# Kernel tuning notes

Measured on AMD Instinct MI355X. Metric: run time of the kernel, lower is better.

Reference implementation:

```python
import jax, jax.numpy as jnp
import numpy as np

SEQ_LEN = 16384
TAG_SIZE = 1024
NEG_INF = -10000.0


def setup_inputs() -> dict:
    key = jax.random.key(0)
    k1, k2, k3 = jax.random.split(key, 3)
    feats = jax.random.normal(k1, (SEQ_LEN, TAG_SIZE), dtype=jnp.float32)
    transitions = jax.random.normal(k2, (TAG_SIZE, TAG_SIZE), dtype=jnp.float32)
    tags = jax.random.randint(k3, (SEQ_LEN,), 0, 1022, dtype=jnp.int64)
    return {
        "feats": feats,
        "transitions": transitions,
        "tags": tags,
        "start_idx": 1022,
        "stop_idx": 1023,
    }


def reference(feats, transitions, tags, start_idx, stop_idx):
    tag_size = transitions.shape[0]

    # --- forward algorithm (log partition function) ---
    init = jnp.full((tag_size,), NEG_INF, dtype=feats.dtype).at[start_idx].set(0.0)

    def step(fv, feat):
        # next_tag_var[j, i] = fv[i] + transitions[j, i] + feat[j]
        new = jax.nn.logsumexp(fv[None, :] + transitions, axis=1) + feat
        return new, None

    fv, _ = jax.lax.scan(step, init, feats)
    forward_score = jax.nn.logsumexp(fv + transitions[stop_idx])  # scalar

    # --- gold score (faithful to original, incl. feats[tags[i+1]] row-indexing) ---
    tags_ext = jnp.concatenate([jnp.array([start_idx], dtype=tags.dtype), tags])
    trans_sum = jnp.sum(transitions[tags_ext[1:], tags_ext[:-1]])  # scalar
    # original adds feats[tags[i+1]] (a full row, [tag_size]) each step -> vector score
    emit_sum = jnp.sum(feats[tags_ext[1:]], axis=0)  # [tag_size]
    gold_score = trans_sum + emit_sum + transitions[stop_idx, tags_ext[-1]]  # [tag_size]

    return forward_score - gold_score  # [tag_size], matches broadcast in torch code
```

## Files before the change

### kernel.cpp

```cpp
#include <hip/hip_runtime.h>
#include <stdint.h>

#define LOG2E_F 1.4426950408889634f
#define LN2_D   0.6931471805599453
#define SEQLEN  16384
#define NTAGS   1024
#define TPB     512
#define NGROUP  32
#define GPB     8
#define ROWS    128
#define CPG     32
#define LSEG    32
#define KCH     512
#define COFF    13.0f
#define GUARD_MAX 100000
#define PARW    (CPG * 256)

typedef float f32x2 __attribute__((ext_vector_type(2)));
typedef float f32x4 __attribute__((ext_vector_type(4)));
typedef uint32_t u32;
typedef uint64_t u64;

#define REP4(M, B)   M(B) M((B)+1) M((B)+2) M((B)+3)
#define REP16(M, B)  REP4(M, B) REP4(M, (B)+4) REP4(M, (B)+8) REP4(M, (B)+12)
#define REP32(M, B)  REP16(M, B) REP16(M, (B)+16)

#if __has_builtin(__builtin_amdgcn_cvt_pk_fp8_f32) && __has_builtin(__builtin_amdgcn_cvt_pk_f32_fp8)
__device__ __forceinline__ u32 pack4_fp8(float x0, float x1, float x2, float x3) {
    int v = __builtin_amdgcn_cvt_pk_fp8_f32(x0, x1, 0, false);
    v = __builtin_amdgcn_cvt_pk_fp8_f32(x2, x3, v, true);
    return (u32)v;
}
__device__ __forceinline__ float dec8(u32 b) {
    f32x2 r = (f32x2)__builtin_amdgcn_cvt_pk_f32_fp8((int)(b & 0xFFu), false);
    return r.x;
}
#else
__device__ __forceinline__ u32 enc1_fp8(float x) {
    if (x >= 448.f) return 0x7Eu;
    if (x < 0.015625f) { int m = (int)(x * 512.f + 0.5f); return (u32)m; }
    u32 u = __float_as_uint(x);
    u += 0x7FFFFu + ((u >> 20) & 1u);
    int e32 = (int)(u >> 23) - 127;
    if (e32 > 8) return 0x7Eu;
    return (u32)(((e32 + 7) << 3) | ((u >> 20) & 7u));
}
__device__ __forceinline__ u32 pack4_fp8(float x0, float x1, float x2, float x3) {
    return enc1_fp8(x0) | (enc1_fp8(x1) << 8) | (enc1_fp8(x2) << 16) | (enc1_fp8(x3) << 24);
}
__device__ __forceinline__ float dec8(u32 b) {
    b &= 0xFFu;
    u32 e = (b >> 3) & 0xFu, m = b & 7u;
    if (e == 0) return (float)m * 0.001953125f;
    return __uint_as_float(((e + 120u) << 23) | (m << 20));
}
#endif

__global__ void crf_prep_k(u32* __restrict__ flags,
                           const float* __restrict__ feats, const int* __restrict__ tags,
                           float* __restrict__ part, const float* __restrict__ trans,
                           const int* __restrict__ start_p, float* __restrict__ tsum) {
    __shared__ int tg[2048];
    __shared__ float red[256];
    const int b = blockIdx.x, tid = threadIdx.x;
    if (b == 0) {
        for (int i = tid; i < NGROUP * 16; i += 256)
            __hip_atomic_store(&flags[i], 0xFFFFu, __ATOMIC_RELAXED, __HIP_MEMORY_SCOPE_AGENT);
    } else if (b < 33) {
        const int bb = b - 1, cch = bb >> 2, jb = bb & 3;
        for (int q = tid; q < 2048; q += 256) tg[q] = tags[cch * 2048 + q];
        __syncthreads();
        const int j = jb * 256 + tid;
        float acc = 0.f;
#pragma unroll 8
        for (int k = 0; k < 2048; ++k) acc += feats[(size_t)tg[k] * NTAGS + j];
        part[cch * NTAGS + j] = acc;
    } else {
        const int start = *start_p;
        float acc = 0.f;
        for (int k = 0; k < 64; ++k) {
            const int t = tid * 64 + k;
            const int prev = (t == 0) ? start : tags[t - 1];
            acc += trans[(size_t)tags[t] * NTAGS + prev];
        }
        red[tid] = acc;
        __syncthreads();
        for (int s = 128; s > 0; s >>= 1) { if (tid < s) red[tid] += red[tid + s]; __syncthreads(); }
        if (tid == 0) *tsum = red[0];
    }
}

__global__ __launch_bounds__(TPB, 1) void crf_scan_k(
    const float* __restrict__ feats, const float* __restrict__ trans,
    u32* __restrict__ wbufs, u32* __restrict__ flags, double* __restrict__ Ssum)
{
    extern __shared__ uint2 wBf[];
    __shared__ u32 cmaxb[2][CPG];
    __shared__ float fbx[8][16][17];
    __shared__ int okf, deadf;

    const int tid = threadIdx.x;
    const int l = tid & 63, wv = tid >> 6;
    const int g = blockIdx.x & 31, rank = blockIdx.x >> 5;
    const int bwd = g >> 4, gl = g & 15;
    const int row0 = rank * ROWS;
    const int pc = tid >> 4, pq = tid & 15;
    const int myc = l & 15, h = l >> 4;
    const int growA = row0 + wv * 16 + myc;
    const int growD = row0 + wv * 16 + h * 4;
    u32* wgrp = wbufs + (size_t)g * (2 * PARW);
    u32* fgrp = flags + g * 16;

    if (tid == 0) { okf = 1; deadf = 0; }
    double Sacc = bwd ? 3.0 : 0.0;

    for (int f = tid; f < CPG * 32; f += TPB) {
        const int c = f >> 5, q = f & 31;
        u32 pk;
        if (!bwd) pk = 0x38383838u;
        else {
            const int t = (gl * CPG + c) * LSEG + LSEG - 1;
            const int j0 = row0 + 4 * q;
            const float4 fv = *(const float4*)&feats[(size_t)t * NTAGS + j0];
            pk = pack4_fp8(exp2f(fv.x * LOG2E_F - 3.0f), exp2f(fv.y * LOG2E_F - 3.0f),
                           exp2f(fv.z * LOG2E_F - 3.0f), exp2f(fv.w * LOG2E_F - 3.0f));
        }
        __hip_atomic_store(&wgrp[c * 256 + (row0 >> 2) + q], pk,
                           __ATOMIC_RELAXED, __HIP_MEMORY_SCOPE_AGENT);
    }
    asm volatile("s_waitcnt vmcnt(0)" ::: "memory");
    __syncthreads();
    if (tid == 0)
        __hip_atomic_store(&fgrp[0 * 8 + rank], 0u, __ATOMIC_RELAXED, __HIP_MEMORY_SCOPE_AGENT);

    u64 afr[32];
#define STG(KK) { \
        const int kb = (KK) * 32 + h * 8; \
        float x0,x1,x2,x3,x4,x5,x6,x7; \
        if (!bwd) { \
            const float4 t0 = *(const float4*)&trans[(size_t)growA * NTAGS + kb]; \
            const float4 t1 = *(const float4*)&trans[(size_t)growA * NTAGS + kb + 4]; \
            x0=t0.x; x1=t0.y; x2=t0.z; x3=t0.w; x4=t1.x; x5=t1.y; x6=t1.z; x7=t1.w; \
        } else { \
            x0 = trans[(size_t)(kb+0)*NTAGS + growA]; x1 = trans[(size_t)(kb+1)*NTAGS + growA]; \
            x2 = trans[(size_t)(kb+2)*NTAGS + growA]; x3 = trans[(size_t)(kb+3)*NTAGS + growA]; \
            x4 = trans[(size_t)(kb+4)*NTAGS + growA]; x5 = trans[(size_t)(kb+5)*NTAGS + growA]; \
            x6 = trans[(size_t)(kb+6)*NTAGS + growA]; x7 = trans[(size_t)(kb+7)*NTAGS + growA]; \
        } \
        const u32 lo = pack4_fp8(exp2f(x0*LOG2E_F), exp2f(x1*LOG2E_F), exp2f(x2*LOG2E_F), exp2f(x3*LOG2E_F)); \
        const u32 hi = pack4_fp8(exp2f(x4*LOG2E_F), exp2f(x5*LOG2E_F), exp2f(x6*LOG2E_F), exp2f(x7*LOG2E_F)); \
        afr[KK] = (u64)lo | ((u64)hi << 32); }
    REP32(STG, 0)
#undef STG

    {
        float av0,av1,av2,av3,av4,av5,av6,av7, bv0,bv1,bv2,bv3,bv4,bv5,bv6,bv7;
#define TV(I) { const int k = h*8 + (I); \
        const float a_ = (float)((myc + k) & 3); \
        const float b_ = (float)(((k ^ myc) & 3) + 1); \
        if ((I)==0){av0=a_;bv0=b_;} if ((I)==1){av1=a_;bv1=b_;} \
        if ((I)==2){av2=a_;bv2=b_;} if ((I)==3){av3=a_;bv3=b_;} \
        if ((I)==4){av4=a_;bv4=b_;} if ((I)==5){av5=a_;bv5=b_;} \
        if ((I)==6){av6=a_;bv6=b_;} if ((I)==7){av7=a_;bv7=b_;} }
        TV(0) TV(1) TV(2) TV(3) TV(4) TV(5) TV(6) TV(7)
#undef TV
        const u64 at = (u64)pack4_fp8(av0,av1,av2,av3) | ((u64)pack4_fp8(av4,av5,av6,av7) << 32);
        const u64 bt = (u64)pack4_fp8(bv0,bv1,bv2,bv3) | ((u64)pack4_fp8(bv4,bv5,bv6,bv7) << 32);
        f32x4 dz = {0.f, 0.f, 0.f, 0.f};
        dz = __builtin_amdgcn_mfma_f32_16x16x32_fp8_fp8((long)at, (long)bt, dz, 0, 0, 0);
        bool good = true;
#pragma unroll
        for (int v = 0; v < 4; ++v) {
            const int row = h * 4 + v;
            float e = 0.f;
            for (int k = 0; k < 32; ++k)
                e += (float)(((row + k) & 3) * (((k ^ myc) & 3) + 1));
            good = good && (dz[v] == e);
        }
        if (!good) okf = 0;
    }
    __syncthreads();
    const bool fb = (okf == 0);

    for (int tau = 0; tau < LSEG; ++tau) {
        const int p = tau & 1;
        const u32 tag = (u32)tau;

        float4 ffa = make_float4(0.f,0.f,0.f,0.f), ffb = make_float4(0.f,0.f,0.f,0.f);
        {
            int t = -1;
            if (!bwd) t = tau; else if (tau <= LSEG - 2) t = LSEG - 2 - tau;
            if (t >= 0) {
                const int ca = gl * CPG + myc;
                ffa = *(const float4*)&feats[(size_t)(ca * LSEG + t) * NTAGS + growD];
                ffb = *(const float4*)&feats[(size_t)((ca + 16) * LSEG + t) * NTAGS + growD];
            }
        }

        if (wv == 0) {
            int guard = 0;
            u32 fv = tag;
            for (;;) {
                if (l < GPB)
                    fv = __hip_atomic_load(&fgrp[p * 8 + l],
                                           __ATOMIC_RELAXED, __HIP_MEMORY_SCOPE_AGENT);
                if (__all(fv == tag)) break;
                if (++guard > GUARD_MAX) { deadf = 1; break; }
            }
        }
        __syncthreads();
        if (deadf) break;

        u32 w[16];
        {
            const u32* pp = wgrp + p * PARW + pc * 256 + pq * 16;
#pragma unroll
            for (int q = 0; q < 8; ++q) {
                const u64 v = __hip_atomic_load((const u64*)(pp + 2 * q),
                                                __ATOMIC_RELAXED, __HIP_MEMORY_SCOPE_AGENT);
                w[2 * q] = (u32)v; w[2 * q + 1] = (u32)(v >> 32);
            }
        }
        {
            const int sb = (pc >> 4) * 64 + (pc & 15);
#pragma unroll
            for (int h2 = 0; h2 < 4; ++h2) {
                wBf[((size_t)p * 32 + 2 * pq)     * 128 + sb + h2 * 16] = make_uint2(w[2*h2],   w[2*h2+1]);
                wBf[((size_t)p * 32 + 2 * pq + 1) * 128 + sb + h2 * 16] = make_uint2(w[8+2*h2], w[9+2*h2]);
            }
        }
        {
            u32 bm = 0;
#pragma unroll
            for (int q = 0; q < 16; ++q) {
                bm = max(bm, w[q] & 0xFFu); bm = max(bm, (w[q] >> 8) & 0xFFu);
                bm = max(bm, (w[q] >> 16) & 0xFFu); bm = max(bm, w[q] >> 24);
            }
#pragma unroll
            for (int o = 8; o > 0; o >>= 1) bm = max(bm, (u32)__shfl_xor((int)bm, o));
            if (pq == 0) cmaxb[p][pc] = bm;
        }
        __syncthreads();

        const float Cme0 = __log2f(dec8(cmaxb[p][myc])) + COFF;
        const float Cme1 = __log2f(dec8(cmaxb[p][16 + myc])) + COFF;
        if (tid < CPG) Sacc += (double)(__log2f(dec8(cmaxb[p][tid])) + COFF);

        f32x4 accA, accB;
        const uint2* wb = &wBf[(size_t)p * 32 * 128];
        if (!fb) {
            f32x4 a0 = {0.f,0.f,0.f,0.f}, a1 = {0.f,0.f,0.f,0.f};
            f32x4 a2 = {0.f,0.f,0.f,0.f}, a3 = {0.f,0.f,0.f,0.f};
#define MF(KK) { const uint2 f0 = wb[(KK)*128 + l]; \
                 const u64 b0 = (u64)f0.x | ((u64)f0.y << 32); \
                 const uint2 f1 = wb[(KK)*128 + 64 + l]; \
                 const u64 b1v = (u64)f1.x | ((u64)f1.y << 32); \
                 if ((KK) & 1) { \
                     a1 = __builtin_amdgcn_mfma_f32_16x16x32_fp8_fp8((long)afr[KK], (long)b0, a1, 0,0,0); \
                     a3 = __builtin_amdgcn_mfma_f32_16x16x32_fp8_fp8((long)afr[KK], (long)b1v, a3, 0,0,0); \
                 } else { \
                     a0 = __builtin_amdgcn_mfma_f32_16x16x32_fp8_fp8((long)afr[KK], (long)b0, a0, 0,0,0); \
                     a2 = __builtin_amdgcn_mfma_f32_16x16x32_fp8_fp8((long)afr[KK], (long)b1v, a2, 0,0,0); \
                 } }
            REP32(MF, 0)
#undef MF
            accA = a0 + a1; accB = a2 + a3;
        } else {
            for (int bt = 0; bt < 2; ++bt) {
                float a16[16];
#pragma unroll
                for (int c = 0; c < 16; ++c) a16[c] = 0.f;
                for (int kk = 0; kk < 32; ++kk) {
                    const u64 av = afr[kk];
                    float ea0 = dec8((u32)av), ea1 = dec8((u32)(av>>8)), ea2 = dec8((u32)(av>>16)), ea3 = dec8((u32)(av>>24));
                    float ea4 = dec8((u32)(av>>32)), ea5 = dec8((u32)(av>>40)), ea6 = dec8((u32)(av>>48)), ea7 = dec8((u32)(av>>56));
#pragma unroll
                    for (int c = 0; c < 16; ++c) {
                        const uint2 bfr = wb[kk * 128 + bt * 64 + h * 16 + c];
                        const u64 bv = (u64)bfr.x | ((u64)bfr.y << 32);
                        float s = fmaf(ea0, dec8((u32)bv), 0.f);
                        s = fmaf(ea1, dec8((u32)(bv>>8)), s);  s = fmaf(ea2, dec8((u32)(bv>>16)), s);
                        s = fmaf(ea3, dec8((u32)(bv>>24)), s); s = fmaf(ea4, dec8((u32)(bv>>32)), s);
                        s = fmaf(ea5, dec8((u32)(bv>>40)), s); s = fmaf(ea6, dec8((u32)(bv>>48)), s);
                        s = fmaf(ea7, dec8((u32)(bv>>56)), s);
                        a16[c] += s;
                    }
                }
#pragma unroll
                for (int c = 0; c < 16; ++c) {
                    float v2 = a16[c];
                    v2 += __shfl_xor(v2, 16); v2 += __shfl_xor(v2, 32);
                    a16[c] = v2;
                }
                if (h == 0) {
#pragma unroll
                    for (int c = 0; c < 16; ++c) fbx[wv][myc][c] = a16[c];
                }
                __syncthreads();
                f32x4 r;
                r.x = fbx[wv][h*4+0][myc]; r.y = fbx[wv][h*4+1][myc];
                r.z = fbx[wv][h*4+2][myc]; r.w = fbx[wv][h*4+3][myc];
                if (bt == 0) accA = r; else accB = r;
                __syncthreads();
            }
        }

        {
            u32* pb = wgrp + (p ^ 1) * PARW;
            const u32 pkA = pack4_fp8(accA.x * exp2f(fmaf(ffa.x, LOG2E_F, -Cme0)),
                                      accA.y * exp2f(fmaf(ffa.y, LOG2E_F, -Cme0)),
                                      accA.z * exp2f(fmaf(ffa.z, LOG2E_F, -Cme0)),
                                      accA.w * exp2f(fmaf(ffa.w, LOG2E_F, -Cme0)));
            const u32 pkB = pack4_fp8(accB.x * exp2f(fmaf(ffb.x, LOG2E_F, -Cme1)),
                                      accB.y * exp2f(fmaf(ffb.y, LOG2E_F, -Cme1)),
                                      accB.z * exp2f(fmaf(ffb.z, LOG2E_F, -Cme1)),
                                      accB.w * exp2f(fmaf(ffb.w, LOG2E_F, -Cme1)));
            __hip_atomic_store(&pb[myc * 256 + (growD >> 2)], pkA,
                               __ATOMIC_RELAXED, __HIP_MEMORY_SCOPE_AGENT);
            __hip_atomic_store(&pb[(16 + myc) * 256 + (growD >> 2)], pkB,
                               __ATOMIC_RELAXED, __HIP_MEMORY_SCOPE_AGENT);
        }
        asm volatile("s_waitcnt vmcnt(0)" ::: "memory");
        __syncthreads();
        if (tid == 0)
            __hip_atomic_store(&fgrp[(p ^ 1) * 8 + rank], tag + 1u,
                               __ATOMIC_RELAXED, __HIP_MEMORY_SCOPE_AGENT);
    }

    if (rank == 0 && tid < CPG)
        Ssum[bwd * KCH + gl * CPG + tid] = Sacc;
}

__global__ void crf_dots_k(const u32* __restrict__ wbufs, const float* __restrict__ trans,
                           const int* __restrict__ start_p, const int* __restrict__ stop_p,
                           double* __restrict__ dotv, double* __restrict__ sumyv,
                           double* __restrict__ finv)
{
    const int c = blockIdx.x;
    const int tid = threadIdx.x;
    __shared__ double red[256];
    const int GRPW = 2 * PARW;
    const u32* y = wbufs + (size_t)(c >> 5) * GRPW + (c & 31) * 256;
    const u32* z = wbufs + (size_t)(16 + (c >> 5)) * GRPW + (c & 31) * 256;
    const u32* ym1 = (c > 0)
        ? (wbufs + (size_t)((c - 1) >> 5) * GRPW + ((c - 1) & 31) * 256) : nullptr;
    const int stop = *stop_p;

    const u32 wy = y[tid];
    double sy = 0, dt = 0, fn = 0;
#pragma unroll
    for (int b = 0; b < 4; ++b) {
        const double yv = (double)dec8(wy >> (8 * b));
        sy += yv;
        if (c == KCH - 1)
            fn += yv * (double)__expf(trans[(size_t)stop * NTAGS + 4 * tid + b]);
    }
    if (c > 0) {
        const u32 wz = z[tid], wm = ym1[tid];
#pragma unroll
        for (int b = 0; b < 4; ++b)
            dt += (double)dec8(wz >> (8 * b)) * (double)dec8(wm >> (8 * b));
    }
    red[tid] = sy; __syncthreads();
    for (int s = 128; s > 0; s >>= 1) { if (tid < s) red[tid] += red[tid + s]; __syncthreads(); }
    if (tid == 0) sumyv[c] = red[0];
    __syncthreads();
    red[tid] = dt; __syncthreads();
    for (int s = 128; s > 0; s >>= 1) { if (tid < s) red[tid] += red[tid + s]; __syncthreads(); }
    if (tid == 0 && c > 0) dotv[c] = red[0];
    __syncthreads();
    red[tid] = fn; __syncthreads();
    for (int s = 128; s > 0; s >>= 1) { if (tid < s) red[tid] += red[tid + s]; __syncthreads(); }
    if (tid == 0 && c == KCH - 1) finv[0] = red[0];
    if (tid == 0 && c == 0) {
        const int st = *start_p;
        dotv[0] = (double)dec8(z[st >> 2] >> (8 * (st & 3)));
    }
}

__global__ void crf_finish_k(const double* __restrict__ Ssum, const double* __restrict__ dotv,
                             const double* __restrict__ sumyv, const double* __restrict__ finv,
                             const float* __restrict__ tsum, const float* __restrict__ part,
                             const float* __restrict__ trans, const int* __restrict__ tags,
                             const int* __restrict__ stop_p, float* __restrict__ out)
{
    __shared__ double red[1024];
    __shared__ float fsv;
    const int tid = threadIdx.x;
    const double* Ssf = Ssum;
    const double* Ssb = Ssum + KCH;
    double t = 0.0;
    if (tid == 0)
        t = log2(dotv[0]) + Ssb[0] - log2(sumyv[0]) - Ssf[0]
          + log2(finv[0]) + Ssf[KCH - 1];
    else if (tid < KCH)
        t = log2(dotv[tid]) + Ssb[tid] + Ssf[tid - 1] - log2(sumyv[tid]) - Ssf[tid];
    red[tid] = t; __syncthreads();
    for (int s = 512; s > 0; s >>= 1) { if (tid < s) red[tid] += red[tid + s]; __syncthreads(); }
    if (tid == 0) fsv = (float)(LN2_D * red[0]);
    __syncthreads();
    float e = 0.f;
    for (int cc = 0; cc < 8; ++cc) e += part[cc * NTAGS + tid];
    const int stop = *stop_p;
    const int last = tags[SEQLEN - 1];
    out[tid] = fsv - (tsum[0] + e + trans[(size_t)stop * NTAGS + last]);
}

extern "C" void kernel_launch(void* const* d_in, const int* in_sizes, int n_in,
                              void* d_out, int out_size, void* d_ws, size_t ws_size,
                              hipStream_t stream) {
    const float* feats = (const float*)d_in[0];
    const float* trans = (const float*)d_in[1];
    const int* tags    = (const int*)d_in[2];
    const int* start_p = (const int*)d_in[3];
    const int* stop_p  = (const int*)d_in[4];
    float* out = (float*)d_out;

    char* ws = (char*)d_ws;
    u32* wbufs    = (u32*)(ws + 0);
    float* part   = (float*)(ws + 2097152);
    double* Ssum  = (double*)(ws + 2129920);
    double* dotv  = (double*)(ws + 2138112);
    double* sumyv = (double*)(ws + 2142208);
    double* finv  = (double*)(ws + 2146304);
    float* tsum   = (float*)(ws + 2146312);
    u32* flags    = (u32*)(ws + 2146816);

    (void)hipFuncSetAttribute((const void*)crf_scan_k,
                              hipFuncAttributeMaxDynamicSharedMemorySize, 65536);

    crf_prep_k<<<34, 256, 0, stream>>>(flags, feats, tags, part, trans, start_p, tsum);
    crf_scan_k<<<NGROUP * GPB, TPB, 65536, stream>>>(feats, trans, wbufs, flags, Ssum);
    crf_dots_k<<<KCH, 256, 0, stream>>>(wbufs, trans, start_p, stop_p, dotv, sumyv, finv);
    crf_finish_k<<<1, 1024, 0, stream>>>(Ssum, dotv, sumyv, finv, tsum, part, trans, tags,
                                         stop_p, out);
}
```

Baseline: 323.9 us.

## Use per-wave cross-block flags, pad LDS stride, move gold-score work after scan

Each wave now publishes its own progress flag, and every wave polls all 64 flags of its group directly. This removes the block-wide barrier before signaling and the single-wave poll followed by a barrier in the per-step chain of the sequential scan. The shared B-fragment buffer uses a padded row stride of 129 to cut LDS bank conflicts. The gold-score gather and transition sum move from the prep kernel into the dots kernel, so the prep kernel only resets flags. The cost is more atomic polling traffic and larger shared memory, and the deadlock flag is now checked only after the later barrier.

```diff
diff --git a/kernel.cpp b/kernel.cpp
--- a/kernel.cpp
+++ b/kernel.cpp
@@ -15,6 +15,7 @@
 #define COFF    13.0f
 #define GUARD_MAX 100000
 #define PARW    (CPG * 256)
+#define KSTRIDE 129
 
 typedef float f32x2 __attribute__((ext_vector_type(2)));
 typedef float f32x4 __attribute__((ext_vector_type(4)));
@@ -56,38 +57,10 @@
 }
 #endif
 
-__global__ void crf_prep_k(u32* __restrict__ flags,
-                           const float* __restrict__ feats, const int* __restrict__ tags,
-                           float* __restrict__ part, const float* __restrict__ trans,
-                           const int* __restrict__ start_p, float* __restrict__ tsum) {
-    __shared__ int tg[2048];
-    __shared__ float red[256];
-    const int b = blockIdx.x, tid = threadIdx.x;
-    if (b == 0) {
-        for (int i = tid; i < NGROUP * 16; i += 256)
-            __hip_atomic_store(&flags[i], 0xFFFFu, __ATOMIC_RELAXED, __HIP_MEMORY_SCOPE_AGENT);
-    } else if (b < 33) {
-        const int bb = b - 1, cch = bb >> 2, jb = bb & 3;
-        for (int q = tid; q < 2048; q += 256) tg[q] = tags[cch * 2048 + q];
-        __syncthreads();
-        const int j = jb * 256 + tid;
-        float acc = 0.f;
-#pragma unroll 8
-        for (int k = 0; k < 2048; ++k) acc += feats[(size_t)tg[k] * NTAGS + j];
-        part[cch * NTAGS + j] = acc;
-    } else {
-        const int start = *start_p;
-        float acc = 0.f;
-        for (int k = 0; k < 64; ++k) {
-            const int t = tid * 64 + k;
-            const int prev = (t == 0) ? start : tags[t - 1];
-            acc += trans[(size_t)tags[t] * NTAGS + prev];
-        }
-        red[tid] = acc;
-        __syncthreads();
-        for (int s = 128; s > 0; s >>= 1) { if (tid < s) red[tid] += red[tid + s]; __syncthreads(); }
-        if (tid == 0) *tsum = red[0];
-    }
+__global__ void crf_prep_k(u32* __restrict__ flags) {
+    const int tid = threadIdx.x;
+    for (int i = tid; i < NGROUP * 128; i += 256)
+        __hip_atomic_store(&flags[i], 0xFFFFu, __ATOMIC_RELAXED, __HIP_MEMORY_SCOPE_AGENT);
 }
 
 __global__ __launch_bounds__(TPB, 1) void crf_scan_k(
@@ -109,7 +82,7 @@
     const int growA = row0 + wv * 16 + myc;
     const int growD = row0 + wv * 16 + h * 4;
     u32* wgrp = wbufs + (size_t)g * (2 * PARW);
-    u32* fgrp = flags + g * 16;
+    u32* fgrp = flags + g * 128;
 
     if (tid == 0) { okf = 1; deadf = 0; }
     double Sacc = bwd ? 3.0 : 0.0;
@@ -129,9 +102,9 @@
                            __ATOMIC_RELAXED, __HIP_MEMORY_SCOPE_AGENT);
     }
     asm volatile("s_waitcnt vmcnt(0)" ::: "memory");
-    __syncthreads();
-    if (tid == 0)
-        __hip_atomic_store(&fgrp[0 * 8 + rank], 0u, __ATOMIC_RELAXED, __HIP_MEMORY_SCOPE_AGENT);
+    if (l == 0)
+        __hip_atomic_store(&fgrp[0 * 64 + rank * 8 + wv], 0u,
+                           __ATOMIC_RELAXED, __HIP_MEMORY_SCOPE_AGENT);
 
     u64 afr[32];
 #define STG(KK) { \
@@ -197,19 +170,15 @@
             }
         }
 
-        if (wv == 0) {
+        {
             int guard = 0;
-            u32 fv = tag;
             for (;;) {
-                if (l < GPB)
-                    fv = __hip_atomic_load(&fgrp[p * 8 + l],
-                                           __ATOMIC_RELAXED, __HIP_MEMORY_SCOPE_AGENT);
+                const u32 fv = __hip_atomic_load(&fgrp[p * 64 + l],
+                                                 __ATOMIC_RELAXED, __HIP_MEMORY_SCOPE_AGENT);
                 if (__all(fv == tag)) break;
                 if (++guard > GUARD_MAX) { deadf = 1; break; }
             }
         }
-        __syncthreads();
-        if (deadf) break;
 
         u32 w[16];
         {
@@ -225,8 +194,8 @@
             const int sb = (pc >> 4) * 64 + (pc & 15);
 #pragma unroll
             for (int h2 = 0; h2 < 4; ++h2) {
-                wBf[((size_t)p * 32 + 2 * pq)     * 128 + sb + h2 * 16] = make_uint2(w[2*h2],   w[2*h2+1]);
-                wBf[((size_t)p * 32 + 2 * pq + 1) * 128 + sb + h2 * 16] = make_uint2(w[8+2*h2], w[9+2*h2]);
+                wBf[((size_t)p * 32 + 2 * pq)     * KSTRIDE + sb + h2 * 16] = make_uint2(w[2*h2],   w[2*h2+1]);
+                wBf[((size_t)p * 32 + 2 * pq + 1) * KSTRIDE + sb + h2 * 16] = make_uint2(w[8+2*h2], w[9+2*h2]);
             }
         }
         {
@@ -241,19 +210,20 @@
             if (pq == 0) cmaxb[p][pc] = bm;
         }
         __syncthreads();
+        if (deadf) break;
 
         const float Cme0 = __log2f(dec8(cmaxb[p][myc])) + COFF;
         const float Cme1 = __log2f(dec8(cmaxb[p][16 + myc])) + COFF;
         if (tid < CPG) Sacc += (double)(__log2f(dec8(cmaxb[p][tid])) + COFF);
 
         f32x4 accA, accB;
-        const uint2* wb = &wBf[(size_t)p * 32 * 128];
+        const uint2* wb = &wBf[(size_t)p * 32 * KSTRIDE];
         if (!fb) {
             f32x4 a0 = {0.f,0.f,0.f,0.f}, a1 = {0.f,0.f,0.f,0.f};
             f32x4 a2 = {0.f,0.f,0.f,0.f}, a3 = {0.f,0.f,0.f,0.f};
-#define MF(KK) { const uint2 f0 = wb[(KK)*128 + l]; \
+#define MF(KK) { const uint2 f0 = wb[(KK)*KSTRIDE + l]; \
                  const u64 b0 = (u64)f0.x | ((u64)f0.y << 32); \
-                 const uint2 f1 = wb[(KK)*128 + 64 + l]; \
+                 const uint2 f1 = wb[(KK)*KSTRIDE + 64 + l]; \
                  const u64 b1v = (u64)f1.x | ((u64)f1.y << 32); \
                  if ((KK) & 1) { \
                      a1 = __builtin_amdgcn_mfma_f32_16x16x32_fp8_fp8((long)afr[KK], (long)b0, a1, 0,0,0); \
@@ -276,7 +246,7 @@
                     float ea4 = dec8((u32)(av>>32)), ea5 = dec8((u32)(av>>40)), ea6 = dec8((u32)(av>>48)), ea7 = dec8((u32)(av>>56));
 #pragma unroll
                     for (int c = 0; c < 16; ++c) {
-                        const uint2 bfr = wb[kk * 128 + bt * 64 + h * 16 + c];
+                        const uint2 bfr = wb[kk * KSTRIDE + bt * 64 + h * 16 + c];
                         const u64 bv = (u64)bfr.x | ((u64)bfr.y << 32);
                         float s = fmaf(ea0, dec8((u32)bv), 0.f);
                         s = fmaf(ea1, dec8((u32)(bv>>8)), s);  s = fmaf(ea2, dec8((u32)(bv>>16)), s);
@@ -321,9 +291,8 @@
                                __ATOMIC_RELAXED, __HIP_MEMORY_SCOPE_AGENT);
         }
         asm volatile("s_waitcnt vmcnt(0)" ::: "memory");
-        __syncthreads();
-        if (tid == 0)
-            __hip_atomic_store(&fgrp[(p ^ 1) * 8 + rank], tag + 1u,
+        if (l == 0)
+            __hip_atomic_store(&fgrp[(p ^ 1) * 64 + rank * 8 + wv], tag + 1u,
                                __ATOMIC_RELAXED, __HIP_MEMORY_SCOPE_AGENT);
     }
 
@@ -332,49 +301,77 @@
 }
 
 __global__ void crf_dots_k(const u32* __restrict__ wbufs, const float* __restrict__ trans,
+                           const float* __restrict__ feats, const int* __restrict__ tags,
                            const int* __restrict__ start_p, const int* __restrict__ stop_p,
                            double* __restrict__ dotv, double* __restrict__ sumyv,
-                           double* __restrict__ finv)
+                           double* __restrict__ finv, float* __restrict__ part,
+                           float* __restrict__ tsum)
 {
+    __shared__ double red[256];
+    __shared__ int tg[2048];
+    __shared__ float redf[256];
     const int c = blockIdx.x;
     const int tid = threadIdx.x;
-    __shared__ double red[256];
-    const int GRPW = 2 * PARW;
-    const u32* y = wbufs + (size_t)(c >> 5) * GRPW + (c & 31) * 256;
-    const u32* z = wbufs + (size_t)(16 + (c >> 5)) * GRPW + (c & 31) * 256;
-    const u32* ym1 = (c > 0)
-        ? (wbufs + (size_t)((c - 1) >> 5) * GRPW + ((c - 1) & 31) * 256) : nullptr;
-    const int stop = *stop_p;
-
-    const u32 wy = y[tid];
-    double sy = 0, dt = 0, fn = 0;
-#pragma unroll
-    for (int b = 0; b < 4; ++b) {
-        const double yv = (double)dec8(wy >> (8 * b));
-        sy += yv;
-        if (c == KCH - 1)
-            fn += yv * (double)__expf(trans[(size_t)stop * NTAGS + 4 * tid + b]);
-    }
-    if (c > 0) {
-        const u32 wz = z[tid], wm = ym1[tid];
-#pragma unroll
-        for (int b = 0; b < 4; ++b)
-            dt += (double)dec8(wz >> (8 * b)) * (double)dec8(wm >> (8 * b));
-    }
-    red[tid] = sy; __syncthreads();
-    for (int s = 128; s > 0; s >>= 1) { if (tid < s) red[tid] += red[tid + s]; __syncthreads(); }
-    if (tid == 0) sumyv[c] = red[0];
-    __syncthreads();
-    red[tid] = dt; __syncthreads();
-    for (int s = 128; s > 0; s >>= 1) { if (tid < s) red[tid] += red[tid + s]; __syncthreads(); }
-    if (tid == 0 && c > 0) dotv[c] = red[0];
-    __syncthreads();
-    red[tid] = fn; __syncthreads();
-    for (int s = 128; s > 0; s >>= 1) { if (tid < s) red[tid] += red[tid + s]; __syncthreads(); }
-    if (tid == 0 && c == KCH - 1) finv[0] = red[0];
-    if (tid == 0 && c == 0) {
-        const int st = *start_p;
-        dotv[0] = (double)dec8(z[st >> 2] >> (8 * (st & 3)));
+
+    if (c < KCH) {
+        const int GRPW = 2 * PARW;
+        const u32* y = wbufs + (size_t)(c >> 5) * GRPW + (c & 31) * 256;
+        const u32* z = wbufs + (size_t)(16 + (c >> 5)) * GRPW + (c & 31) * 256;
+        const u32* ym1 = (c > 0)
+            ? (wbufs + (size_t)((c - 1) >> 5) * GRPW + ((c - 1) & 31) * 256) : nullptr;
+        const int stop = *stop_p;
+
+        const u32 wy = y[tid];
+        double sy = 0, dt = 0, fn = 0;
+#pragma unroll
+        for (int b = 0; b < 4; ++b) {
+            const double yv = (double)dec8(wy >> (8 * b));
+            sy += yv;
+            if (c == KCH - 1)
+                fn += yv * (double)__expf(trans[(size_t)stop * NTAGS + 4 * tid + b]);
+        }
+        if (c > 0) {
+            const u32 wz = z[tid], wm = ym1[tid];
+#pragma unroll
+            for (int b = 0; b < 4; ++b)
+                dt += (double)dec8(wz >> (8 * b)) * (double)dec8(wm >> (8 * b));
+        }
+        red[tid] = sy; __syncthreads();
+        for (int s = 128; s > 0; s >>= 1) { if (tid < s) red[tid] += red[tid + s]; __syncthreads(); }
+        if (tid == 0) sumyv[c] = red[0];
+        __syncthreads();
+        red[tid] = dt; __syncthreads();
+        for (int s = 128; s > 0; s >>= 1) { if (tid < s) red[tid] += red[tid + s]; __syncthreads(); }
+        if (tid == 0 && c > 0) dotv[c] = red[0];
+        __syncthreads();
+        red[tid] = fn; __syncthreads();
+        for (int s = 128; s > 0; s >>= 1) { if (tid < s) red[tid] += red[tid + s]; __syncthreads(); }
+        if (tid == 0 && c == KCH - 1) finv[0] = red[0];
+        if (tid == 0 && c == 0) {
+            const int st = *start_p;
+            dotv[0] = (double)dec8(z[st >> 2] >> (8 * (st & 3)));
+        }
+    } else if (c < KCH + 32) {
+        const int bb = c - KCH, cch = bb >> 2, jb = bb & 3;
+        for (int q = tid; q < 2048; q += 256) tg[q] = tags[cch * 2048 + q];
+        __syncthreads();
+        const int j = jb * 256 + tid;
+        float acc = 0.f;
+#pragma unroll 8
+        for (int k = 0; k < 2048; ++k) acc += feats[(size_t)tg[k] * NTAGS + j];
+        part[cch * NTAGS + j] = acc;
+    } else {
+        const int start = *start_p;
+        float acc = 0.f;
+        for (int k = 0; k < 64; ++k) {
+            const int t = tid * 64 + k;
+            const int prev = (t == 0) ? start : tags[t - 1];
+            acc += trans[(size_t)tags[t] * NTAGS + prev];
+        }
+        redf[tid] = acc;
+        __syncthreads();
+        for (int s = 128; s > 0; s >>= 1) { if (tid < s) redf[tid] += redf[tid + s]; __syncthreads(); }
+        if (tid == 0) *tsum = redf[0];
     }
 }
 
@@ -427,11 +424,14 @@
     u32* flags    = (u32*)(ws + 2146816);
 
     (void)hipFuncSetAttribute((const void*)crf_scan_k,
-                              hipFuncAttributeMaxDynamicSharedMemorySize, 65536);
-
-    crf_prep_k<<<34, 256, 0, stream>>>(flags, feats, tags, part, trans, start_p, tsum);
-    crf_scan_k<<<NGROUP * GPB, TPB, 65536, stream>>>(feats, trans, wbufs, flags, Ssum);
-    crf_dots_k<<<KCH, 256, 0, stream>>>(wbufs, trans, start_p, stop_p, dotv, sumyv, finv);
+                              hipFuncAttributeMaxDynamicSharedMemorySize,
+                              2 * 32 * KSTRIDE * 8);
+
+    crf_prep_k<<<1, 256, 0, stream>>>(flags);
+    crf_scan_k<<<NGROUP * GPB, TPB, 2 * 32 * KSTRIDE * 8, stream>>>(feats, trans, wbufs,
+                                                                    flags, Ssum);
+    crf_dots_k<<<KCH + 33, 256, 0, stream>>>(wbufs, trans, feats, tags, start_p, stop_p,
+                                             dotv, sumyv, finv, part, tsum);
     crf_finish_k<<<1, 1024, 0, stream>>>(Ssum, dotv, sumyv, finv, tsum, part, trans, tags,
                                          stop_p, out);
 }
```

After: 494.7 us. +52.7%, slower.

## Fold gold-score prep into scan kernel as extra blocks and pad LDS stride

Applied to the files above, without the earlier changes.

Moves the emission-sum and transition-sum gold-score work from the prep kernel into 17 extra blocks of the scan kernel, so this work overlaps the long sequential scan instead of running before it. The prep kernel now only resets the flags. The LDS row stride for the B operand staging goes from 128 to 129 uint2 to reduce bank conflicts on the strided writes. Risks: the extra blocks take CUs alongside the persistent scan blocks, which could matter if the spin-waiting groups need all blocks co-resident, and the padding changes the LDS read pattern for the MFMA loads.

```diff
diff --git a/kernel.cpp b/kernel.cpp
--- a/kernel.cpp
+++ b/kernel.cpp
@@ -15,6 +15,8 @@
 #define COFF    13.0f
 #define GUARD_MAX 100000
 #define PARW    (CPG * 256)
+#define KSTRIDE 129
+#define NAUX    17
 
 typedef float f32x2 __attribute__((ext_vector_type(2)));
 typedef float f32x4 __attribute__((ext_vector_type(4)));
@@ -56,43 +58,17 @@
 }
 #endif
 
-__global__ void crf_prep_k(u32* __restrict__ flags,
-                           const float* __restrict__ feats, const int* __restrict__ tags,
-                           float* __restrict__ part, const float* __restrict__ trans,
-                           const int* __restrict__ start_p, float* __restrict__ tsum) {
-    __shared__ int tg[2048];
-    __shared__ float red[256];
-    const int b = blockIdx.x, tid = threadIdx.x;
-    if (b == 0) {
-        for (int i = tid; i < NGROUP * 16; i += 256)
-            __hip_atomic_store(&flags[i], 0xFFFFu, __ATOMIC_RELAXED, __HIP_MEMORY_SCOPE_AGENT);
-    } else if (b < 33) {
-        const int bb = b - 1, cch = bb >> 2, jb = bb & 3;
-        for (int q = tid; q < 2048; q += 256) tg[q] = tags[cch * 2048 + q];
-        __syncthreads();
-        const int j = jb * 256 + tid;
-        float acc = 0.f;
-#pragma unroll 8
-        for (int k = 0; k < 2048; ++k) acc += feats[(size_t)tg[k] * NTAGS + j];
-        part[cch * NTAGS + j] = acc;
-    } else {
-        const int start = *start_p;
-        float acc = 0.f;
-        for (int k = 0; k < 64; ++k) {
-            const int t = tid * 64 + k;
-            const int prev = (t == 0) ? start : tags[t - 1];
-            acc += trans[(size_t)tags[t] * NTAGS + prev];
-        }
-        red[tid] = acc;
-        __syncthreads();
-        for (int s = 128; s > 0; s >>= 1) { if (tid < s) red[tid] += red[tid + s]; __syncthreads(); }
-        if (tid == 0) *tsum = red[0];
-    }
+__global__ void crf_prep_k(u32* __restrict__ flags) {
+    const int tid = threadIdx.x;
+    for (int i = tid; i < NGROUP * 16; i += 256)
+        __hip_atomic_store(&flags[i], 0xFFFFu, __ATOMIC_RELAXED, __HIP_MEMORY_SCOPE_AGENT);
 }
 
 __global__ __launch_bounds__(TPB, 1) void crf_scan_k(
     const float* __restrict__ feats, const float* __restrict__ trans,
-    u32* __restrict__ wbufs, u32* __restrict__ flags, double* __restrict__ Ssum)
+    const int* __restrict__ tags, const int* __restrict__ start_p,
+    u32* __restrict__ wbufs, u32* __restrict__ flags, double* __restrict__ Ssum,
+    float* __restrict__ part, float* __restrict__ tsum)
 {
     extern __shared__ uint2 wBf[];
     __shared__ u32 cmaxb[2][CPG];
@@ -100,6 +76,40 @@
     __shared__ int okf, deadf;
 
     const int tid = threadIdx.x;
+
+    if (blockIdx.x >= NGROUP * GPB) {
+        const int bb = blockIdx.x - NGROUP * GPB;
+        u32* ldsraw = (u32*)wBf;
+        if (bb < 16) {
+            int* tg = (int*)ldsraw;
+            const int cch = bb >> 1, jb = bb & 1;
+            for (int q = tid; q < 2048; q += TPB) tg[q] = tags[cch * 2048 + q];
+            __syncthreads();
+            const int j = jb * 512 + tid;
+            float acc = 0.f;
+#pragma unroll 8
+            for (int k = 0; k < 2048; ++k) acc += feats[(size_t)tg[k] * NTAGS + j];
+            part[cch * NTAGS + j] = acc;
+        } else {
+            float* red = (float*)ldsraw;
+            const int start = *start_p;
+            float acc = 0.f;
+            for (int k = 0; k < 32; ++k) {
+                const int t = tid * 32 + k;
+                const int prev = (t == 0) ? start : tags[t - 1];
+                acc += trans[(size_t)tags[t] * NTAGS + prev];
+            }
+            red[tid] = acc;
+            __syncthreads();
+            for (int s = 256; s > 0; s >>= 1) {
+                if (tid < s) red[tid] += red[tid + s];
+                __syncthreads();
+            }
+            if (tid == 0) *tsum = red[0];
+        }
+        return;
+    }
+
     const int l = tid & 63, wv = tid >> 6;
     const int g = blockIdx.x & 31, rank = blockIdx.x >> 5;
     const int bwd = g >> 4, gl = g & 15;
@@ -108,6 +118,7 @@
     const int myc = l & 15, h = l >> 4;
     const int growA = row0 + wv * 16 + myc;
     const int growD = row0 + wv * 16 + h * 4;
+    const int sb = (pc >> 4) * 64 + (pc & 15);
     u32* wgrp = wbufs + (size_t)g * (2 * PARW);
     u32* fgrp = flags + g * 16;
 
@@ -222,11 +233,10 @@
             }
         }
         {
-            const int sb = (pc >> 4) * 64 + (pc & 15);
 #pragma unroll
             for (int h2 = 0; h2 < 4; ++h2) {
-                wBf[((size_t)p * 32 + 2 * pq)     * 128 + sb + h2 * 16] = make_uint2(w[2*h2],   w[2*h2+1]);
-                wBf[((size_t)p * 32 + 2 * pq + 1) * 128 + sb + h2 * 16] = make_uint2(w[8+2*h2], w[9+2*h2]);
+                wBf[((size_t)p * 32 + 2 * pq)     * KSTRIDE + sb + h2 * 16] = make_uint2(w[2*h2],   w[2*h2+1]);
+                wBf[((size_t)p * 32 + 2 * pq + 1) * KSTRIDE + sb + h2 * 16] = make_uint2(w[8+2*h2], w[9+2*h2]);
             }
         }
         {
@@ -247,13 +257,13 @@
         if (tid < CPG) Sacc += (double)(__log2f(dec8(cmaxb[p][tid])) + COFF);
 
         f32x4 accA, accB;
-        const uint2* wb = &wBf[(size_t)p * 32 * 128];
+        const uint2* wb = &wBf[(size_t)p * 32 * KSTRIDE];
         if (!fb) {
             f32x4 a0 = {0.f,0.f,0.f,0.f}, a1 = {0.f,0.f,0.f,0.f};
             f32x4 a2 = {0.f,0.f,0.f,0.f}, a3 = {0.f,0.f,0.f,0.f};
-#define MF(KK) { const uint2 f0 = wb[(KK)*128 + l]; \
+#define MF(KK) { const uint2 f0 = wb[(KK)*KSTRIDE + l]; \
                  const u64 b0 = (u64)f0.x | ((u64)f0.y << 32); \
-                 const uint2 f1 = wb[(KK)*128 + 64 + l]; \
+                 const uint2 f1 = wb[(KK)*KSTRIDE + 64 + l]; \
                  const u64 b1v = (u64)f1.x | ((u64)f1.y << 32); \
                  if ((KK) & 1) { \
                      a1 = __builtin_amdgcn_mfma_f32_16x16x32_fp8_fp8((long)afr[KK], (long)b0, a1, 0,0,0); \
@@ -276,7 +286,7 @@
                     float ea4 = dec8((u32)(av>>32)), ea5 = dec8((u32)(av>>40)), ea6 = dec8((u32)(av>>48)), ea7 = dec8((u32)(av>>56));
 #pragma unroll
                     for (int c = 0; c < 16; ++c) {
-                        const uint2 bfr = wb[kk * 128 + bt * 64 + h * 16 + c];
+                        const uint2 bfr = wb[kk * KSTRIDE + bt * 64 + h * 16 + c];
                         const u64 bv = (u64)bfr.x | ((u64)bfr.y << 32);
                         float s = fmaf(ea0, dec8((u32)bv), 0.f);
                         s = fmaf(ea1, dec8((u32)(bv>>8)), s);  s = fmaf(ea2, dec8((u32)(bv>>16)), s);
@@ -427,10 +437,12 @@
     u32* flags    = (u32*)(ws + 2146816);
 
     (void)hipFuncSetAttribute((const void*)crf_scan_k,
-                              hipFuncAttributeMaxDynamicSharedMemorySize, 65536);
-
-    crf_prep_k<<<34, 256, 0, stream>>>(flags, feats, tags, part, trans, start_p, tsum);
-    crf_scan_k<<<NGROUP * GPB, TPB, 65536, stream>>>(feats, trans, wbufs, flags, Ssum);
+                              hipFuncAttributeMaxDynamicSharedMemorySize,
+                              2 * 32 * KSTRIDE * 8);
+
+    crf_prep_k<<<1, 256, 0, stream>>>(flags);
+    crf_scan_k<<<NGROUP * GPB + NAUX, TPB, 2 * 32 * KSTRIDE * 8, stream>>>(
+        feats, trans, tags, start_p, wbufs, flags, Ssum, part, tsum);
     crf_dots_k<<<KCH, 256, 0, stream>>>(wbufs, trans, start_p, stop_p, dotv, sumyv, finv);
     crf_finish_k<<<1, 1024, 0, stream>>>(Ssum, dotv, sumyv, finv, tsum, part, trans, tags,
                                          stop_p, out);
```

New measurement: 346.0 us. +6.8%, slower.
